# Kernel tuning notes

Measured on AMD Instinct MI355X. Metric: run time of the kernel, lower is better.

Reference implementation:

```python
import jax, jax.numpy as jnp
import numpy as np

EPS = 1e-5


def conv2d(x, w, b):
    out = jax.lax.conv_general_dilated(x, w, window_strides=(1, 1), padding=((1, 1), (1, 1)),
                                       dimension_numbers=('NCHW', 'OIHW', 'NCHW'))
    return out + b[None, :, None, None]


def batchnorm_train(x, gamma, beta):
    # training-mode BN: batch statistics over (N, H, W)
    mean = jnp.mean(x, axis=(0, 2, 3), keepdims=True)
    var = jnp.var(x, axis=(0, 2, 3), keepdims=True)
    return gamma[None, :, None, None] * (x - mean) * jax.lax.rsqrt(var + EPS) + beta[None, :, None, None]


def maxpool2(x):
    return jax.lax.reduce_window(x, -jnp.inf, jax.lax.max, (1, 1, 2, 2), (1, 1, 2, 2), 'VALID')


def rls(Phi, y, W, P):
    # sequential recursive-least-squares over samples; W: [D+1, C], P: [D+1, D+1]
    def step(carry, inp):
        W, P = carry
        xi, yi = inp                    # xi: [129], yi: [10]
        Px = P @ xi                     # [129]
        denom = 1.0 + xi @ Px           # scalar
        err = yi - xi @ W               # [10]
        W = W + jnp.outer(Px, err) / denom
        P = P - jnp.outer(Px, xi @ P) / denom
        return (W, P), None
    (W, P), _ = jax.lax.scan(step, (W, P), (Phi, y))
    return W, P


def cnn_features(x, conv1_w, conv1_b, bn1_g, bn1_b, conv2_w, conv2_b, bn2_g, bn2_b, fc1_w, fc1_b):
    h = maxpool2(jax.nn.relu(batchnorm_train(conv2d(x, conv1_w, conv1_b), bn1_g, bn1_b)))   # [B,32,14,14]
    h = maxpool2(jax.nn.relu(batchnorm_train(conv2d(h, conv2_w, conv2_b), bn2_g, bn2_b)))   # [B,64,7,7]
    h = h.reshape(h.shape[0], 64 * 7 * 7)
    return jax.nn.relu(h @ fc1_w.T + fc1_b)                                                 # [B,128]


def setup_inputs() -> dict:
    key = jax.random.key(0)
    ks = jax.random.split(key, 8)
    B = 4096
    x = jax.random.normal(ks[0], (B, 1, 28, 28), dtype=jnp.float32)
    y = jax.random.uniform(ks[1], (B, 10), dtype=jnp.float32)
    conv1_w = jax.random.normal(ks[2], (32, 1, 3, 3), dtype=jnp.float32) * 0.3
    conv2_w = jax.random.normal(ks[3], (64, 32, 3, 3), dtype=jnp.float32) * 0.06
    fc1_w = jax.random.normal(ks[4], (128, 3136), dtype=jnp.float32) * 0.02
    W_rls = jax.random.normal(ks[5], (129, 10), dtype=jnp.float32) * 0.05
    P_rls = jnp.eye(129, dtype=jnp.float32)
    return {
        'x': x, 'y': y,
        'conv1_w': conv1_w, 'conv1_b': jnp.full((32,), 0.01, jnp.float32),
        'bn1_g': jnp.ones((32,), jnp.float32), 'bn1_b': jnp.zeros((32,), jnp.float32),
        'conv2_w': conv2_w, 'conv2_b': jnp.full((64,), 0.01, jnp.float32),
        'bn2_g': jnp.ones((64,), jnp.float32), 'bn2_b': jnp.zeros((64,), jnp.float32),
        'fc1_w': fc1_w, 'fc1_b': jnp.full((128,), 0.01, jnp.float32),
        'W_rls': W_rls, 'P_rls': P_rls,
        'separate': 1,
    }


def reference(x, y, conv1_w, conv1_b, bn1_g, bn1_b, conv2_w, conv2_b, bn2_g, bn2_b,
              fc1_w, fc1_b, W_rls, P_rls, separate):
    feature = cnn_features(x, conv1_w, conv1_b, bn1_g, bn1_b,
                           conv2_w, conv2_b, bn2_g, bn2_b, fc1_w, fc1_b)   # [B,128]
    if separate:
        Phi = jnp.concatenate([feature, jnp.ones((feature.shape[0], 1), feature.dtype)], axis=1)  # [B,129]
        W_new, P_new = rls(Phi, y, W_rls, P_rls)
        W_new = jax.lax.stop_gradient(W_new)  # torch updates under no_grad
    else:
        W_new = W_rls
    # final_layer with (possibly) RLS-updated weights: weight = W_new[:-1].T, bias = W_new[-1]
    return feature @ W_new[:-1] + W_new[-1]
```

## Files before the change

kernel.cpp:

```cpp
#include <hip/hip_runtime.h>
#include <math.h>

#define TPB 256
#define EPSBN 1e-5f
#define PW 16

typedef __attribute__((ext_vector_type(8))) short bf8v;
typedef __attribute__((ext_vector_type(4))) float f4v;

static __device__ __forceinline__ unsigned short f2bf(float f) {
    union { float f; unsigned u; } v; v.f = f;
    unsigned r = v.u + 0x7fffu + ((v.u >> 16) & 1u);
    return (unsigned short)(r >> 16);
}
static __device__ __forceinline__ float rdl(float v, int l) {
    return __int_as_float(__builtin_amdgcn_readlane(__float_as_int(v), l));
}

#define WS_WAG      0u
#define WS_FWP      9216u
#define WS_SC1      209920u
#define WS_SH1      209952u
#define WS_SCK      209984u
#define WS_SHK      213120u
#define WS_G        216256u
#define WS_C        232897u
#define WS_WNEW     234187u
#define WS_BN1PART  235520u
#define WS_BN2PART  497664u
#define WS_PHI      1021952u
#define WS_FPART    1550336u
#define WS_GPART    5220352u
#define WS_CPART    7399936u
#define WS_PMAX     7598080u
#define WS_PMINH    20443136u
#define WS_TOTAL    26865664ull

__global__ __launch_bounds__(TPB) void kWk1(const float* __restrict__ w2,
                                            const float* __restrict__ fw,
                                            const float* __restrict__ x,
                                            unsigned* __restrict__ wAg_u,
                                            unsigned* __restrict__ fwp_u,
                                            float* __restrict__ qpart) {
    __shared__ float xs[900];
    __shared__ float red[4][54];
    if (blockIdx.x < 820) {
        int e = blockIdx.x * TPB + threadIdx.x;
        if (e < 9216) {
            int jj = e & 3, lane = (e >> 2) & 63, mt = (e >> 8) & 3, t = e >> 10;
            int j0 = jj * 2;
            int co = mt * 16 + (lane & 15);
            int ci = (lane >> 4) * 8 + j0;
            unsigned h0 = f2bf(w2[(co * 32 + ci) * 9 + t]);
            unsigned h1 = f2bf(w2[(co * 32 + ci + 1) * 9 + t]);
            wAg_u[e] = h0 | (h1 << 16);
        } else if (e < 9216 + 200704) {
            int f = e - 9216;
            int kk = (f & 15) * 2, n = (f >> 4) & 127, g = f >> 11;
            unsigned h0 = f2bf(fw[n * 3136 + g * 32 + kk]);
            unsigned h1 = f2bf(fw[n * 3136 + g * 32 + kk + 1]);
            fwp_u[f] = h0 | (h1 << 16);
        }
        return;
    }
    int bid = blockIdx.x - 820;
    int tid = threadIdx.x;
    float acc[54];
#pragma unroll
    for (int i = 0; i < 54; ++i) acc[i] = 0.f;
    for (int img = 0; img < 16; ++img) {
        int n = bid * 16 + img;
        for (int i = tid; i < 900; i += TPB) xs[i] = 0.f;
        __syncthreads();
        for (int i = tid; i < 784; i += TPB) {
            int r = i / 28, c = i % 28;
            xs[(r + 1) * 30 + (c + 1)] = x[n * 784 + i];
        }
        __syncthreads();
        for (int p = tid; p < 784; p += TPB) {
            int oy = p / 28, ox = p % 28;
            float v[9];
#pragma unroll
            for (int t = 0; t < 9; ++t) v[t] = xs[(oy + t / 3) * 30 + ox + (t % 3)];
            int qi = 9;
#pragma unroll
            for (int t = 0; t < 9; ++t) {
                acc[t] += v[t];
#pragma unroll
                for (int u = t; u < 9; ++u) acc[qi++] += v[t] * v[u];
            }
        }
        __syncthreads();
    }
    int wv = tid >> 6, lane = tid & 63;
#pragma unroll
    for (int i = 0; i < 54; ++i) {
        float s = acc[i];
        for (int d = 1; d < 64; d <<= 1) s += __shfl_xor(s, d);
        if (lane == 0) red[wv][i] = s;
    }
    __syncthreads();
    if (tid < 54)
        qpart[bid * 54 + tid] = red[0][tid] + red[1][tid] + red[2][tid] + red[3][tid];
}

__global__ __launch_bounds__(64) void k2_bn1_final(const float* __restrict__ qpart,
                                                   const float* __restrict__ w1,
                                                   const float* __restrict__ g1,
                                                   const float* __restrict__ be1,
                                                   float* __restrict__ sc1,
                                                   float* __restrict__ sh1) {
    __shared__ float T[54];
    int tid = threadIdx.x;
    if (tid < 54) {
        float s = 0.f;
#pragma unroll 8
        for (int b = 0; b < 256; ++b) s += qpart[b * 54 + tid];
        T[tid] = s;
    }
    __syncthreads();
    if (tid < 32) {
        const float inv = 1.f / (4096.f * 784.f);
        float w[9];
#pragma unroll
        for (int t = 0; t < 9; ++t) w[t] = w1[tid * 9 + t];
        float mean = 0.f;
#pragma unroll
        for (int t = 0; t < 9; ++t) mean += w[t] * T[t];
        mean *= inv;
        float ex2 = 0.f;
        int qi = 9;
#pragma unroll
        for (int t = 0; t < 9; ++t)
#pragma unroll
            for (int u = t; u < 9; ++u) {
                float c = w[t] * w[u] * T[qi++];
                ex2 += (u == t) ? c : 2.f * c;
            }
        ex2 *= inv;
        float var = ex2 - mean * mean;
        float a = g1[tid] * rsqrtf(var + EPSBN);
        sc1[tid] = a;
        sh1[tid] = be1[tid] - a * mean;
    }
}

__global__ __launch_bounds__(TPB) void k34_conv2_mfma(const float* __restrict__ x,
                                                      const float* __restrict__ w1,
                                                      const float* __restrict__ sc1,
                                                      const float* __restrict__ sh1,
                                                      const unsigned short* __restrict__ wAg,
                                                      const float* __restrict__ b2,
                                                      float* __restrict__ pmax,
                                                      float* __restrict__ bn2part) {
    __shared__ __align__(16) unsigned short SH[14992];
    float* xs   = (float*)(SH + 13056);
    float* wred = (float*)(SH + 13056);
    float* b2l  = (float*)(SH + 14856);
    float* slab = (float*)SH;

    int tid = threadIdx.x;
    int n   = blockIdx.x;
    int lane = tid & 63, wv = tid >> 6, quad = lane >> 4, l15 = lane & 15;

    for (int i = tid; i < 5120; i += TPB) ((unsigned*)SH)[i] = 0u;
    for (int i = tid; i < 900; i += TPB) xs[i] = 0.f;
    if (tid < 64) b2l[tid] = b2[tid];
    __syncthreads();
    for (int i = tid; i < 784; i += TPB) {
        int r = i / 28, c = i % 28;
        xs[(r + 1) * 30 + (c + 1)] = x[n * 784 + i];
    }
    __syncthreads();

    if (tid < 196) {
        int py = tid / 14, px = tid % 14;
        int paddr = (py + 1) * 16 + (px + 1);
        float patch[4][4];
#pragma unroll
        for (int r = 0; r < 4; ++r)
#pragma unroll
            for (int c = 0; c < 4; ++c) patch[r][c] = xs[(2 * py + r) * 30 + 2 * px + c];
        unsigned hp0 = 0, hp1 = 0;
#pragma unroll
        for (int co = 0; co < 32; ++co) {
            float a = sc1[co], cc = sh1[co];
            float m = -1e30f;
#pragma unroll
            for (int sy = 0; sy < 2; ++sy)
#pragma unroll
                for (int sx = 0; sx < 2; ++sx) {
                    float v = 0.f;
#pragma unroll
                    for (int t = 0; t < 9; ++t) v += patch[sy + t / 3][sx + t % 3] * w1[co * 9 + t];
                    m = fmaxf(m, v);
                }
            unsigned short h = f2bf(fmaxf(a * m + cc, 0.f));
            int q = co & 3;
            if (q == 0) hp0 = h;
            else if (q == 1) hp0 |= (unsigned)h << 16;
            else if (q == 2) hp1 = h;
            else {
                hp1 |= (unsigned)h << 16;
                *(uint2*)((unsigned*)SH + paddr * 20 + ((co - 3) >> 1)) = make_uint2(hp0, hp1);
            }
        }
    }
    __syncthreads();

    int baseB[4];
    float vmsk[4];
    int pvals[4];
#pragma unroll
    for (int i = 0; i < 4; ++i) {
        int nt = wv + 4 * i;
        int p  = nt * 16 + l15;
        vmsk[i]  = (nt <= 12 && p < 196) ? 1.f : 0.f;
        pvals[i] = p;
        int pc = p < 196 ? p : 195;
        int py = pc / 14, px = pc - py * 14;
        baseB[i] = ((py + 1) * 16 + (px + 1)) * 80 + quad * 16;
    }
    f4v acc[4][4];
#pragma unroll
    for (int i = 0; i < 4; ++i)
#pragma unroll
        for (int mt = 0; mt < 4; ++mt) acc[i][mt] = (f4v){0.f, 0.f, 0.f, 0.f};

    const char* h1hiB = (const char*)SH;
#pragma unroll
    for (int t = 0; t < 9; ++t) {
        const int toff = ((t / 3) - 1) * 1280 + ((t % 3) - 1) * 80;
        bf8v wa0 = *(const bf8v*)(wAg + ((t * 4 + 0) * 64 + lane) * 8);
        bf8v wa1 = *(const bf8v*)(wAg + ((t * 4 + 1) * 64 + lane) * 8);
        bf8v wa2 = *(const bf8v*)(wAg + ((t * 4 + 2) * 64 + lane) * 8);
        bf8v wa3 = *(const bf8v*)(wAg + ((t * 4 + 3) * 64 + lane) * 8);
#pragma unroll
        for (int i = 0; i < 4; ++i) {
            if (wv + 4 * i > 12) continue;
            bf8v bhi = *(const bf8v*)(h1hiB + baseB[i] + toff);
            acc[i][0] = __builtin_amdgcn_mfma_f32_16x16x32_bf16(wa0, bhi, acc[i][0], 0, 0, 0);
            acc[i][1] = __builtin_amdgcn_mfma_f32_16x16x32_bf16(wa1, bhi, acc[i][1], 0, 0, 0);
            acc[i][2] = __builtin_amdgcn_mfma_f32_16x16x32_bf16(wa2, bhi, acc[i][2], 0, 0, 0);
            acc[i][3] = __builtin_amdgcn_mfma_f32_16x16x32_bf16(wa3, bhi, acc[i][3], 0, 0, 0);
        }
    }
    float bb[4][4];
#pragma unroll
    for (int mt = 0; mt < 4; ++mt)
#pragma unroll
        for (int r = 0; r < 4; ++r) bb[mt][r] = b2l[mt * 16 + quad * 4 + r];
#pragma unroll
    for (int i = 0; i < 4; ++i)
#pragma unroll
        for (int mt = 0; mt < 4; ++mt)
#pragma unroll
            for (int r = 0; r < 4; ++r) acc[i][mt][r] += bb[mt][r];
    float ss[4][4], qq[4][4];
#pragma unroll
    for (int mt = 0; mt < 4; ++mt)
#pragma unroll
        for (int r = 0; r < 4; ++r) { ss[mt][r] = 0.f; qq[mt][r] = 0.f; }
#pragma unroll
    for (int i = 0; i < 4; ++i) {
        if (wv + 4 * i > 12) continue;
#pragma unroll
        for (int mt = 0; mt < 4; ++mt)
#pragma unroll
            for (int r = 0; r < 4; ++r) {
                float v = acc[i][mt][r] * vmsk[i];
                ss[mt][r] += v;
                qq[mt][r] += v * v;
            }
    }
#pragma unroll
    for (int d = 1; d < 16; d <<= 1)
#pragma unroll
        for (int mt = 0; mt < 4; ++mt)
#pragma unroll
            for (int r = 0; r < 4; ++r) {
                ss[mt][r] += __shfl_xor(ss[mt][r], d);
                qq[mt][r] += __shfl_xor(qq[mt][r], d);
            }
    __syncthreads();
    if (l15 == 0) {
#pragma unroll
        for (int mt = 0; mt < 4; ++mt)
#pragma unroll
            for (int r = 0; r < 4; ++r) {
                int co = mt * 16 + quad * 4 + r;
                wred[wv * 64 + co]        = ss[mt][r];
                wred[256 + wv * 64 + co]  = qq[mt][r];
            }
    }
    __syncthreads();
    if (tid < 64) {
        float s = wred[tid] + wred[64 + tid] + wred[128 + tid] + wred[192 + tid];
        float q = wred[256 + tid] + wred[320 + tid] + wred[384 + tid] + wred[448 + tid];
        bn2part[(n * 64 + tid) * 2 + 0] = s;
        bn2part[(n * 64 + tid) * 2 + 1] = q;
    }
    int pk = tid >> 3, pj = tid & 7;
#pragma unroll
    for (int c2 = 0; c2 < 2; ++c2) {
        __syncthreads();
#pragma unroll
        for (int mtl = 0; mtl < 2; ++mtl) {
            int mt = c2 * 2 + mtl;
#pragma unroll
            for (int i = 0; i < 4; ++i) {
                if (wv + 4 * i > 12) continue;
                if (vmsk[i] > 0.f) {
#pragma unroll
                    for (int r = 0; r < 4; ++r)
                        slab[(mtl * 16 + quad * 4 + r) * 204 + pvals[i]] = acc[i][mt][r];
                }
            }
        }
        __syncthreads();
        {
            int j7 = (pj >= 7) ? 1 : 0;
            int qy = j7, qx = pj - 7 * j7;
            size_t obase = (size_t)n * 3136 + (c2 * 32 + pk) * 49;
            const float* srow = slab + pk * 204;
#pragma unroll
            for (int it = 0; it < 7; ++it) {
                int pp = pj + (it << 3);
                if (pp < 49) {
                    int p0 = qy * 28 + qx * 2;
                    float2 a01 = *(const float2*)(srow + p0);
                    float2 a23 = *(const float2*)(srow + p0 + 14);
                    float mx = fmaxf(fmaxf(a01.x, a01.y), fmaxf(a23.x, a23.y));
                    pmax[obase + pp] = mx;
                }
                qx += 1; qy += 1;
                if (qx >= 7) { qx -= 7; qy += 1; }
            }
        }
    }
}

__global__ __launch_bounds__(TPB) void k5_bn2_final(const float* __restrict__ bn2part,
                                                    const float* __restrict__ g2,
                                                    const float* __restrict__ be2,
                                                    float* __restrict__ sck,
                                                    float* __restrict__ shk) {
    __shared__ float red[TPB][2];
    __shared__ float sAC[2];
    int tid = threadIdx.x, co = blockIdx.x;
    float s = 0.f, q = 0.f;
    for (int i = tid; i < 4096; i += TPB) {
        s += bn2part[(i * 64 + co) * 2 + 0];
        q += bn2part[(i * 64 + co) * 2 + 1];
    }
    red[tid][0] = s; red[tid][1] = q;
    __syncthreads();
    for (int off = TPB / 2; off; off >>= 1) {
        if (tid < off) { red[tid][0] += red[tid + off][0]; red[tid][1] += red[tid + off][1]; }
        __syncthreads();
    }
    if (tid == 0) {
        const float count = 4096.f * 196.f;
        float mean = red[0][0] / count;
        float var  = red[0][1] / count - mean * mean;
        float a    = g2[co] * rsqrtf(var + EPSBN);
        sAC[0] = a;
        sAC[1] = be2[co] - a * mean;
    }
    __syncthreads();
    if (tid < 49) {
        sck[co * 49 + tid] = sAC[0];
        shk[co * 49 + tid] = sAC[1];
    }
}

__global__ __launch_bounds__(TPB) void k7_fc1_mfma(const float* __restrict__ pmax,
                                                   const float* __restrict__ sck,
                                                   const float* __restrict__ shk,
                                                   const unsigned short* __restrict__ fwp,
                                                   float* __restrict__ fpart) {
    __shared__ __align__(16) unsigned short K7S[7680];
    unsigned short* Ahi = K7S;
    unsigned short* Bsl = K7S + 2560;
    int tid = threadIdx.x;
    int mt = blockIdx.x & 63, ks = blockIdx.x >> 6;
    int m0 = mt * 64;
    int lane = tid & 63, wv = tid >> 6, quad = lane >> 4, l15 = lane & 15;
    f4v acc[8];
#pragma unroll
    for (int i = 0; i < 8; ++i) acc[i] = (f4v){0.f, 0.f, 0.f, 0.f};

    for (int it = 0; it < 14; ++it) {
        int g  = ks * 14 + it;
        int k0 = g * 32;
#pragma unroll
        for (int i = 0; i < 8; ++i) {
            int e  = tid + i * TPB;
            int r  = e >> 5, kk = e & 31;
            int k  = k0 + kk;
            float a = sck[k], c = shk[k];
            size_t src = (size_t)(m0 + r) * 3136 + k;
            float v = fmaxf(a * pmax[src] + c, 0.f);
            Ahi[r * 40 + kk] = f2bf(v);
        }
        {
            const uint4* src = (const uint4*)(fwp + (size_t)g * 4096 + tid * 16);
            uint4 w0 = src[0], w1 = src[1];
            int n = tid >> 1, kk0 = (tid & 1) * 16;
            *(uint4*)(Bsl + n * 40 + kk0)     = w0;
            *(uint4*)(Bsl + n * 40 + kk0 + 8) = w1;
        }
        __syncthreads();
        bf8v ahi = *(const bf8v*)(Ahi + (wv * 16 + l15) * 40 + quad * 8);
#pragma unroll
        for (int nt = 0; nt < 8; ++nt) {
            bf8v b = *(const bf8v*)(Bsl + (nt * 16 + l15) * 40 + quad * 8);
            acc[nt] = __builtin_amdgcn_mfma_f32_16x16x32_bf16(ahi, b, acc[nt], 0, 0, 0);
        }
        __syncthreads();
    }
#pragma unroll
    for (int nt = 0; nt < 8; ++nt)
#pragma unroll
        for (int r = 0; r < 4; ++r) {
            int m = m0 + wv * 16 + quad * 4 + r;
            int nn = nt * 16 + l15;
            fpart[(size_t)ks * 524288 + m * 128 + nn] = acc[nt][r];
        }
}

__global__ __launch_bounds__(TPB) void k7b_relu(const float* __restrict__ fpart,
                                                const float* __restrict__ fb,
                                                float* __restrict__ Phi) {
    int e = blockIdx.x * TPB + threadIdx.x;
    int n = e >> 7, f = e & 127;
    float s = fb[f];
#pragma unroll
    for (int c = 0; c < 7; ++c) s += fpart[(size_t)c * 524288 + e];
    Phi[n * 129 + f] = fmaxf(s, 0.f);
    if (f == 0) Phi[n * 129 + 128] = 1.0f;
}

__global__ __launch_bounds__(TPB) void k8_gram(const float* __restrict__ Phi,
                                               const float* __restrict__ y,
                                               float* __restrict__ Gpart,
                                               float* __restrict__ Cpart) {
    __shared__ __align__(16) float ph[32 * 132];
    __shared__ __align__(16) float yl[32 * 12];
    int tid = threadIdx.x;
    int cB  = blockIdx.x;
    int n0  = cB * 32;
    for (int i = tid; i < 32 * 132; i += TPB) ph[i] = 0.f;
    for (int i = tid; i < 32 * 12; i += TPB) yl[i] = 0.f;
    __syncthreads();
    for (int i = tid; i < 32 * 129; i += TPB) {
        int r = i / 129, d = i % 129;
        ph[r * 132 + d] = Phi[(n0 + r) * 129 + d];
    }
    for (int i = tid; i < 320; i += TPB) {
        int r = i / 10, j = i % 10;
        yl[r * 12 + j] = y[(n0 + r) * 10 + j];
    }
    __syncthreads();
    for (int g = tid; g < 129 * 33; g += TPB) {
        int i = g / 33, j0 = (g % 33) * 4;
        float4 s = make_float4(0.f, 0.f, 0.f, 0.f);
        for (int r = 0; r < 32; ++r) {
            float  vi = ph[r * 132 + i];
            float4 vj = *(const float4*)&ph[r * 132 + j0];
            s.x += vi * vj.x; s.y += vi * vj.y; s.z += vi * vj.z; s.w += vi * vj.w;
        }
        *(float4*)&Gpart[(size_t)cB * 17028 + i * 132 + j0] = s;
    }
    for (int g = tid; g < 129 * 3; g += TPB) {
        int i = g / 3, j0 = (g % 3) * 4;
        float4 s = make_float4(0.f, 0.f, 0.f, 0.f);
        for (int r = 0; r < 32; ++r) {
            float  vi = ph[r * 132 + i];
            float4 vj = *(const float4*)&yl[r * 12 + j0];
            s.x += vi * vj.x; s.y += vi * vj.y; s.z += vi * vj.z; s.w += vi * vj.w;
        }
        *(float4*)&Cpart[(size_t)cB * 1548 + i * 12 + j0] = s;
    }
}

__global__ __launch_bounds__(TPB) void k9_reduce(const float* __restrict__ Gpart,
                                                 const float* __restrict__ Cpart,
                                                 float* __restrict__ G,
                                                 float* __restrict__ C) {
    int e = blockIdx.x * TPB + threadIdx.x;
    if (e < 16641) {
        int i = e / 129, j = e % 129;
        float s = 0.f;
        for (int c = 0; c < 128; ++c) s += Gpart[(size_t)c * 17028 + i * 132 + j];
        G[e] = s;
    } else if (e < 16641 + 1290) {
        int e2 = e - 16641;
        int i = e2 / 10, j = e2 % 10;
        float s = 0.f;
        for (int c = 0; c < 128; ++c) s += Cpart[(size_t)c * 1548 + i * 12 + j];
        C[e2] = s;
    }
}

__global__ __launch_bounds__(TPB) void k10_solve(const float* __restrict__ G,
                                                 const float* __restrict__ C,
                                                 const float* __restrict__ W0,
                                                 float* __restrict__ Wnew) {
    __shared__ __align__(16) float M[129 * 140];
    __shared__ __align__(16) float LpT[PW * 116];
    __shared__ float L11s[PW * 16];
    __shared__ float invD[129];
    __shared__ float x128s[10];
    int tid = threadIdx.x;
    int lane = tid & 63, wv = tid >> 6;
    for (int e = tid; e < 129 * 129; e += TPB) {
        int i = e / 129, j = e % 129;
        M[i * 140 + j] = G[e] + (i == j ? 1.f : 0.f);
    }
    for (int i = tid; i < 129; i += TPB) M[i * 140 + 129] = 0.f;
    for (int e = tid; e < 1290; e += TPB) {
        int i = e / 10, c = e % 10;
        M[i * 140 + 130 + c] = W0[e] + C[e];
    }
    __syncthreads();

    for (int k0 = 0; k0 < 128; k0 += PW) {
        const int kend = k0 + PW;
        if (wv == 0) {
            bool act = lane < PW;
            int r  = k0 + lane;
            int rc = act ? r : k0;
            float u[PW], Lr[PW];
#pragma unroll
            for (int j = 0; j < PW; ++j) u[j] = M[rc * 140 + k0 + j];
            float dval = u[0];
#pragma unroll
            for (int k = 0; k < PW; ++k) {
                if (lane == k) dval = u[k];
                float piv = rdl(u[k], k);
                float f   = u[k] * __builtin_amdgcn_rcpf(piv);
                float fm  = (act && lane > k) ? f : 0.f;
                Lr[k] = fm;
#pragma unroll
                for (int j = 0; j < PW; ++j)
                    if (j > k) u[j] -= fm * rdl(u[j], k);
            }
            if (act) {
#pragma unroll
                for (int j = 0; j < PW; ++j)
                    if (j >= lane) M[r * 140 + k0 + j] = u[j];
#pragma unroll
                for (int k = 0; k < PW; ++k)
                    if (k < lane) L11s[k * 16 + lane] = Lr[k];
                invD[r] = __builtin_amdgcn_rcpf(dval);
            }
        }
        __syncthreads();
        if (tid < 128) {
            int cidx = tid;
            if (cidx < 113) {
                int r = cidx < k0 ? cidx : cidx + PW;
                float4 a4[4];
#pragma unroll
                for (int q = 0; q < 4; ++q) a4[q] = *(const float4*)&M[r * 140 + k0 + q * 4];
                float a[PW];
#pragma unroll
                for (int q = 0; q < 4; ++q) {
                    a[q * 4 + 0] = a4[q].x; a[q * 4 + 1] = a4[q].y;
                    a[q * 4 + 2] = a4[q].z; a[q * 4 + 3] = a4[q].w;
                }
#pragma unroll
                for (int k = 0; k < PW; ++k)
                    LpT[k * 116 + cidx] = a[k] * invD[k0 + k];
            }
        } else {
            int j = kend + (tid - 128);
            if (j < 140) {
                float yv[PW];
#pragma unroll
                for (int kk = 0; kk < PW; ++kk) {
                    float v = M[(k0 + kk) * 140 + j];
#pragma unroll
                    for (int m = 0; m < PW; ++m)
                        if (m < kk) v -= L11s[m * 16 + kk] * yv[m];
                    yv[kk] = v;
                }
                float xv[PW];
#pragma unroll
                for (int kk = PW - 1; kk >= 0; --kk) {
                    float v = yv[kk];
#pragma unroll
                    for (int m = 0; m < PW; ++m)
                        if (m > kk) v -= M[(k0 + kk) * 140 + k0 + m] * xv[m];
                    M[(k0 + kk) * 140 + j] = v;
                    xv[kk] = v * invD[k0 + kk];
                }
            }
        }
        __syncthreads();
        const int Jn = 140 - kend;
        const int nrt = 29, nct = Jn >> 2;
        for (int t = tid; t < nrt * nct; t += TPB) {
            int tr = t % nrt, tc = t / nrt;
            int c0 = tr * 4;
            int j0 = kend + tc * 4;
            float4 s0 = {0, 0, 0, 0}, s1 = {0, 0, 0, 0}, s2 = {0, 0, 0, 0}, s3 = {0, 0, 0, 0};
#pragma unroll
            for (int kk = 0; kk < PW; ++kk) {
                float4 L4 = *(const float4*)&LpT[kk * 116 + c0];
                float4 U4 = *(const float4*)&M[(k0 + kk) * 140 + j0];
                s0.x += L4.x * U4.x; s0.y += L4.x * U4.y; s0.z += L4.x * U4.z; s0.w += L4.x * U4.w;
                s1.x += L4.y * U4.x; s1.y += L4.y * U4.y; s1.z += L4.y * U4.z; s1.w += L4.y * U4.w;
                s2.x += L4.z * U4.x; s2.y += L4.z * U4.y; s2.z += L4.z * U4.z; s2.w += L4.z * U4.w;
                s3.x += L4.w * U4.x; s3.y += L4.w * U4.y; s3.z += L4.w * U4.z; s3.w += L4.w * U4.w;
            }
            float4 sv[4] = {s0, s1, s2, s3};
#pragma unroll
            for (int i = 0; i < 4; ++i) {
                int cidx = c0 + i;
                if (cidx < 113) {
                    int r = cidx < k0 ? cidx : cidx + PW;
                    float4 mv = *(const float4*)&M[r * 140 + j0];
                    mv.x -= sv[i].x; mv.y -= sv[i].y; mv.z -= sv[i].z; mv.w -= sv[i].w;
                    *(float4*)&M[r * 140 + j0] = mv;
                }
            }
        }
        __syncthreads();
    }
    if (tid == 0) {
        float i128 = __builtin_amdgcn_rcpf(M[128 * 140 + 128]);
#pragma unroll
        for (int c = 0; c < 10; ++c) x128s[c] = M[128 * 140 + 130 + c] * i128;
    }
    __syncthreads();
    if (tid < 128) {
        int r = tid;
        float m128 = M[r * 140 + 128];
        float idr  = invD[r];
#pragma unroll
        for (int c = 0; c < 10; ++c)
            Wnew[r * 10 + c] = (M[r * 140 + 130 + c] - m128 * x128s[c]) * idr;
    } else if (tid == 128) {
#pragma unroll
        for (int c = 0; c < 10; ++c) Wnew[1280 + c] = x128s[c];
    }
}

__global__ __launch_bounds__(TPB) void k11_out(const float* __restrict__ Phi,
                                               const float* __restrict__ Wnew,
                                               float* __restrict__ out) {
    __shared__ float Wl[1290];
    int tid = threadIdx.x;
    for (int i = tid; i < 1290; i += TPB) Wl[i] = Wnew[i];
    __syncthreads();
    int idx = blockIdx.x * TPB + tid;
    int n = idx / 10, j = idx % 10;
    float s = 0.f;
    for (int d = 0; d < 129; ++d) s += Phi[n * 129 + d] * Wl[d * 10 + j];
    out[idx] = s;
}

extern "C" void kernel_launch(void* const* d_in, const int* in_sizes, int n_in,
                              void* d_out, int out_size, void* d_ws, size_t ws_size,
                              hipStream_t stream) {
    const float* x   = (const float*)d_in[0];
    const float* y   = (const float*)d_in[1];
    const float* w1  = (const float*)d_in[2];
    const float* g1  = (const float*)d_in[4];
    const float* be1 = (const float*)d_in[5];
    const float* w2  = (const float*)d_in[6];
    const float* b2  = (const float*)d_in[7];
    const float* g2  = (const float*)d_in[8];
    const float* be2 = (const float*)d_in[9];
    const float* fw  = (const float*)d_in[10];
    const float* fb  = (const float*)d_in[11];
    const float* W0  = (const float*)d_in[12];
    float* out = (float*)d_out;
    float* ws  = (float*)d_ws;
    if (ws_size < WS_TOTAL * 4ull) return;

    unsigned* wAg_u = (unsigned*)(ws + WS_WAG);
    unsigned* fwp_u = (unsigned*)(ws + WS_FWP);
    const unsigned short* wAg_h = (const unsigned short*)wAg_u;
    const unsigned short* fwp_h = (const unsigned short*)fwp_u;
    float* sc1     = ws + WS_SC1;
    float* sh1     = ws + WS_SH1;
    float* sck     = ws + WS_SCK;
    float* shk     = ws + WS_SHK;
    float* G       = ws + WS_G;
    float* C       = ws + WS_C;
    float* Wnew    = ws + WS_WNEW;
    float* qpart   = ws + WS_BN1PART;
    float* bn2part = ws + WS_BN2PART;
    float* Phi     = ws + WS_PHI;
    float* fpart   = ws + WS_FPART;
    float* Gpart   = ws + WS_GPART;
    float* Cpart   = ws + WS_CPART;
    float* pmax    = ws + WS_PMAX;

    kWk1<<<1076, TPB, 0, stream>>>(w2, fw, x, wAg_u, fwp_u, qpart);
    k2_bn1_final<<<1, 64, 0, stream>>>(qpart, w1, g1, be1, sc1, sh1);
    k34_conv2_mfma<<<4096, TPB, 0, stream>>>(x, w1, sc1, sh1, wAg_h, b2, pmax, bn2part);
    k5_bn2_final<<<64, TPB, 0, stream>>>(bn2part, g2, be2, sck, shk);
    k7_fc1_mfma<<<448, TPB, 0, stream>>>(pmax, sck, shk, fwp_h, fpart);
    k7b_relu<<<2048, TPB, 0, stream>>>(fpart, fb, Phi);
    k8_gram<<<128, TPB, 0, stream>>>(Phi, y, Gpart, Cpart);
    k9_reduce<<<71, TPB, 0, stream>>>(Gpart, Cpart, G, C);
    k10_solve<<<1, TPB, 0, stream>>>(G, C, W0, Wnew);
    k11_out<<<160, TPB, 0, stream>>>(Phi, Wnew, out);
}
```

Baseline: 375.5 us.

## Split conv2 MFMA into two channel halves to cut accumulator registers

The conv2 kernel now computes the 64 output channels in two passes of 32. Each pass runs its own MFMA loop, bias add, BN-stat reduction and pool write. This halves the live accumulator array (acc[4][4] becomes acc2[4][2]), which should lower VGPR pressure and may allow more waves per CU. In exchange, the h1 tile is read from LDS twice. LDS is rearranged so h1 sits separate from the slab buffer and no longer aliases it; the footprint grows from about 30KB to about 48KB per block, which could limit blocks per CU.

```diff
diff --git a/kernel.cpp b/kernel.cpp
--- a/kernel.cpp
+++ b/kernel.cpp
@@ -153,17 +153,19 @@
                                                       const float* __restrict__ b2,
                                                       float* __restrict__ pmax,
                                                       float* __restrict__ bn2part) {
-    __shared__ __align__(16) unsigned short SH[14992];
-    float* xs   = (float*)(SH + 13056);
-    float* wred = (float*)(SH + 13056);
-    float* b2l  = (float*)(SH + 14856);
+    __shared__ __align__(16) unsigned short SH[24192];
     float* slab = (float*)SH;
+    float* xs   = (float*)SH;
+    unsigned* H1u = (unsigned*)(SH + 12800);
+    const char* h1hiB = (const char*)(SH + 12800);
+    float* wred = (float*)(SH + 23040);
+    float* b2l  = (float*)(SH + 24064);
 
     int tid = threadIdx.x;
     int n   = blockIdx.x;
     int lane = tid & 63, wv = tid >> 6, quad = lane >> 4, l15 = lane & 15;
 
-    for (int i = tid; i < 5120; i += TPB) ((unsigned*)SH)[i] = 0u;
+    for (int i = tid; i < 5120; i += TPB) H1u[i] = 0u;
     for (int i = tid; i < 900; i += TPB) xs[i] = 0.f;
     if (tid < 64) b2l[tid] = b2[tid];
     __syncthreads();
@@ -202,7 +204,7 @@
             else if (q == 2) hp1 = h;
             else {
                 hp1 |= (unsigned)h << 16;
-                *(uint2*)((unsigned*)SH + paddr * 20 + ((co - 3) >> 1)) = make_uint2(hp0, hp1);
+                *(uint2*)(H1u + paddr * 20 + ((co - 3) >> 1)) = make_uint2(hp0, hp1);
             }
         }
     }
@@ -221,99 +223,84 @@
         int py = pc / 14, px = pc - py * 14;
         baseB[i] = ((py + 1) * 16 + (px + 1)) * 80 + quad * 16;
     }
-    f4v acc[4][4];
-#pragma unroll
-    for (int i = 0; i < 4; ++i)
-#pragma unroll
-        for (int mt = 0; mt < 4; ++mt) acc[i][mt] = (f4v){0.f, 0.f, 0.f, 0.f};
-
-    const char* h1hiB = (const char*)SH;
-#pragma unroll
-    for (int t = 0; t < 9; ++t) {
-        const int toff = ((t / 3) - 1) * 1280 + ((t % 3) - 1) * 80;
-        bf8v wa0 = *(const bf8v*)(wAg + ((t * 4 + 0) * 64 + lane) * 8);
-        bf8v wa1 = *(const bf8v*)(wAg + ((t * 4 + 1) * 64 + lane) * 8);
-        bf8v wa2 = *(const bf8v*)(wAg + ((t * 4 + 2) * 64 + lane) * 8);
-        bf8v wa3 = *(const bf8v*)(wAg + ((t * 4 + 3) * 64 + lane) * 8);
+
+    int pk = tid >> 3, pj = tid & 7;
+
+#pragma unroll
+    for (int c2 = 0; c2 < 2; ++c2) {
+        f4v acc2[4][2];
+#pragma unroll
+        for (int i = 0; i < 4; ++i)
+#pragma unroll
+            for (int mtl = 0; mtl < 2; ++mtl) acc2[i][mtl] = (f4v){0.f, 0.f, 0.f, 0.f};
+#pragma unroll
+        for (int t = 0; t < 9; ++t) {
+            const int toff = ((t / 3) - 1) * 1280 + ((t % 3) - 1) * 80;
+            bf8v wa0 = *(const bf8v*)(wAg + ((t * 4 + c2 * 2 + 0) * 64 + lane) * 8);
+            bf8v wa1 = *(const bf8v*)(wAg + ((t * 4 + c2 * 2 + 1) * 64 + lane) * 8);
+#pragma unroll
+            for (int i = 0; i < 4; ++i) {
+                if (wv + 4 * i > 12) continue;
+                bf8v bhi = *(const bf8v*)(h1hiB + baseB[i] + toff);
+                acc2[i][0] = __builtin_amdgcn_mfma_f32_16x16x32_bf16(wa0, bhi, acc2[i][0], 0, 0, 0);
+                acc2[i][1] = __builtin_amdgcn_mfma_f32_16x16x32_bf16(wa1, bhi, acc2[i][1], 0, 0, 0);
+            }
+        }
+#pragma unroll
+        for (int mtl = 0; mtl < 2; ++mtl) {
+            float bb[4];
+#pragma unroll
+            for (int r = 0; r < 4; ++r) bb[r] = b2l[(c2 * 2 + mtl) * 16 + quad * 4 + r];
+#pragma unroll
+            for (int i = 0; i < 4; ++i)
+#pragma unroll
+                for (int r = 0; r < 4; ++r) acc2[i][mtl][r] += bb[r];
+        }
+        float ss[2][4], qq[2][4];
+#pragma unroll
+        for (int mtl = 0; mtl < 2; ++mtl)
+#pragma unroll
+            for (int r = 0; r < 4; ++r) { ss[mtl][r] = 0.f; qq[mtl][r] = 0.f; }
 #pragma unroll
         for (int i = 0; i < 4; ++i) {
             if (wv + 4 * i > 12) continue;
-            bf8v bhi = *(const bf8v*)(h1hiB + baseB[i] + toff);
-            acc[i][0] = __builtin_amdgcn_mfma_f32_16x16x32_bf16(wa0, bhi, acc[i][0], 0, 0, 0);
-            acc[i][1] = __builtin_amdgcn_mfma_f32_16x16x32_bf16(wa1, bhi, acc[i][1], 0, 0, 0);
-            acc[i][2] = __builtin_amdgcn_mfma_f32_16x16x32_bf16(wa2, bhi, acc[i][2], 0, 0, 0);
-            acc[i][3] = __builtin_amdgcn_mfma_f32_16x16x32_bf16(wa3, bhi, acc[i][3], 0, 0, 0);
-        }
-    }
-    float bb[4][4];
-#pragma unroll
-    for (int mt = 0; mt < 4; ++mt)
-#pragma unroll
-        for (int r = 0; r < 4; ++r) bb[mt][r] = b2l[mt * 16 + quad * 4 + r];
-#pragma unroll
-    for (int i = 0; i < 4; ++i)
-#pragma unroll
-        for (int mt = 0; mt < 4; ++mt)
-#pragma unroll
-            for (int r = 0; r < 4; ++r) acc[i][mt][r] += bb[mt][r];
-    float ss[4][4], qq[4][4];
-#pragma unroll
-    for (int mt = 0; mt < 4; ++mt)
-#pragma unroll
-        for (int r = 0; r < 4; ++r) { ss[mt][r] = 0.f; qq[mt][r] = 0.f; }
-#pragma unroll
-    for (int i = 0; i < 4; ++i) {
-        if (wv + 4 * i > 12) continue;
-#pragma unroll
-        for (int mt = 0; mt < 4; ++mt)
-#pragma unroll
-            for (int r = 0; r < 4; ++r) {
-                float v = acc[i][mt][r] * vmsk[i];
-                ss[mt][r] += v;
-                qq[mt][r] += v * v;
-            }
-    }
-#pragma unroll
-    for (int d = 1; d < 16; d <<= 1)
-#pragma unroll
-        for (int mt = 0; mt < 4; ++mt)
-#pragma unroll
-            for (int r = 0; r < 4; ++r) {
-                ss[mt][r] += __shfl_xor(ss[mt][r], d);
-                qq[mt][r] += __shfl_xor(qq[mt][r], d);
-            }
-    __syncthreads();
-    if (l15 == 0) {
-#pragma unroll
-        for (int mt = 0; mt < 4; ++mt)
-#pragma unroll
-            for (int r = 0; r < 4; ++r) {
-                int co = mt * 16 + quad * 4 + r;
-                wred[wv * 64 + co]        = ss[mt][r];
-                wred[256 + wv * 64 + co]  = qq[mt][r];
-            }
-    }
-    __syncthreads();
-    if (tid < 64) {
-        float s = wred[tid] + wred[64 + tid] + wred[128 + tid] + wred[192 + tid];
-        float q = wred[256 + tid] + wred[320 + tid] + wred[384 + tid] + wred[448 + tid];
-        bn2part[(n * 64 + tid) * 2 + 0] = s;
-        bn2part[(n * 64 + tid) * 2 + 1] = q;
-    }
-    int pk = tid >> 3, pj = tid & 7;
-#pragma unroll
-    for (int c2 = 0; c2 < 2; ++c2) {
-        __syncthreads();
+#pragma unroll
+            for (int mtl = 0; mtl < 2; ++mtl)
+#pragma unroll
+                for (int r = 0; r < 4; ++r) {
+                    float v = acc2[i][mtl][r] * vmsk[i];
+                    ss[mtl][r] += v;
+                    qq[mtl][r] += v * v;
+                }
+        }
+#pragma unroll
+        for (int d = 1; d < 16; d <<= 1)
+#pragma unroll
+            for (int mtl = 0; mtl < 2; ++mtl)
+#pragma unroll
+                for (int r = 0; r < 4; ++r) {
+                    ss[mtl][r] += __shfl_xor(ss[mtl][r], d);
+                    qq[mtl][r] += __shfl_xor(qq[mtl][r], d);
+                }
+        if (l15 == 0) {
+#pragma unroll
+            for (int mtl = 0; mtl < 2; ++mtl)
+#pragma unroll
+                for (int r = 0; r < 4; ++r) {
+                    int co = (c2 * 2 + mtl) * 16 + quad * 4 + r;
+                    wred[wv * 64 + co]       = ss[mtl][r];
+                    wred[256 + wv * 64 + co] = qq[mtl][r];
+                }
+        }
 #pragma unroll
         for (int mtl = 0; mtl < 2; ++mtl) {
-            int mt = c2 * 2 + mtl;
 #pragma unroll
             for (int i = 0; i < 4; ++i) {
                 if (wv + 4 * i > 12) continue;
                 if (vmsk[i] > 0.f) {
 #pragma unroll
                     for (int r = 0; r < 4; ++r)
-                        slab[(mtl * 16 + quad * 4 + r) * 204 + pvals[i]] = acc[i][mt][r];
+                        slab[(mtl * 16 + quad * 4 + r) * 200 + pvals[i]] = acc2[i][mtl][r];
                 }
             }
         }
@@ -322,7 +309,7 @@
             int j7 = (pj >= 7) ? 1 : 0;
             int qy = j7, qx = pj - 7 * j7;
             size_t obase = (size_t)n * 3136 + (c2 * 32 + pk) * 49;
-            const float* srow = slab + pk * 204;
+            const float* srow = slab + pk * 200;
 #pragma unroll
             for (int it = 0; it < 7; ++it) {
                 int pp = pj + (it << 3);
@@ -337,6 +324,13 @@
                 if (qx >= 7) { qx -= 7; qy += 1; }
             }
         }
+        __syncthreads();
+    }
+    if (tid < 64) {
+        float s = wred[tid] + wred[64 + tid] + wred[128 + tid] + wred[192 + tid];
+        float q = wred[256 + tid] + wred[320 + tid] + wred[384 + tid] + wred[448 + tid];
+        bn2part[(n * 64 + tid) * 2 + 0] = s;
+        bn2part[(n * 64 + tid) * 2 + 1] = q;
     }
 }
 
```

Result: faster. 360.5 us (-4.0%).
